# Optimization experiments

Hardware: AMD Instinct MI355X
Metric: run time of the kernel (lower is better)

## Reference

```python
import jax, jax.numpy as jnp
import numpy as np

B, C, H, W = 32, 512, 32, 32
R = C // 2  # reduced channels for key/prod projections


def setup_inputs() -> dict:
    key = jax.random.key(0)
    ks = jax.random.split(key, 8)
    s_in = 1.0 / np.sqrt(C)
    return {
        "x": jax.random.normal(ks[0], (B, C, H, W), jnp.float32),
        "Wk": jax.random.normal(ks[1], (R, C), jnp.float32) * s_in,
        "bk": jax.random.normal(ks[2], (R,), jnp.float32) * s_in,
        "Wp": jax.random.normal(ks[3], (R, C), jnp.float32) * s_in,
        "bp": jax.random.normal(ks[4], (R,), jnp.float32) * s_in,
        "Wv": jax.random.normal(ks[5], (C, C), jnp.float32) * s_in,
        "bv": jax.random.normal(ks[6], (C,), jnp.float32) * s_in,
        "param": jax.random.normal(ks[7], (1,), jnp.float32),
    }


def _conv1x1(x, Wmat, b):
    # 1x1 conv on NCHW == per-pixel channel matmul
    return jnp.einsum('bchw,oc->bohw', x, Wmat) + b[None, :, None, None]


def reference(x, Wk, bk, Wp, bp, Wv, bv, param):
    b, c, h, w = x.shape
    hw = h * w
    f_key = _conv1x1(x, Wk, bk).reshape(b, -1, hw).transpose(0, 2, 1)  # [B,HW,R]
    f_prod = _conv1x1(x, Wp, bp).reshape(b, -1, hw)                    # [B,R,HW]
    f_value = _conv1x1(x, Wv, bv).reshape(b, -1, hw)                   # [B,C,HW]
    energy = jnp.einsum('bnr,brm->bnm', f_key, f_prod)                 # [B,HW,HW]
    similarity = jax.nn.softmax(energy, axis=-1)
    # bmm(f_value, similarity^T): out[b,c,n] = sum_m f_value[b,c,m] * sim[b,n,m]
    attended = jnp.einsum('bcm,bnm->bcn', f_value, similarity).reshape(b, c, h, w)
    return x + attended * param
```

## Files before the change

kernel.cpp:

```cpp
#include <hip/hip_runtime.h>
#include <hip/hip_bf16.h>

#define BATCH 32
#define CCH   512
#define HWSZ  1024
#define RCH   256

typedef __attribute__((ext_vector_type(8))) _Float16 f16x8;
typedef __attribute__((ext_vector_type(4))) float f32x4;

__device__ __forceinline__ ushort f2h(float f) {
    _Float16 h = (_Float16)f;
    ushort u; __builtin_memcpy(&u, &h, 2);
    return u;
}
__device__ __forceinline__ float h2f(ushort u) {
    _Float16 h; __builtin_memcpy(&h, &u, 2);
    return (float)h;
}

__device__ __forceinline__ void load_lds16(const void* g, void* l) {
    __builtin_amdgcn_global_load_lds((const __attribute__((address_space(1))) void*)g,
                                     (__attribute__((address_space(3))) void*)l,
                                     16, 0, 0);
}

__device__ __forceinline__ void xcd_swizzle(int& bx, int& by, int& bz) {
    int gx = gridDim.x, gy = gridDim.y;
    int n   = gx * gy * gridDim.z;
    int lin = bx + gx * (by + gy * bz);
    int cpx = n >> 3;
    int s = (lin & 7) * cpx + (lin >> 3);
    bx = s % gx; s /= gx;
    by = s % gy;
    bz = s / gy;
}

__global__ __launch_bounds__(256) void k_pre(
    const float* __restrict__ x, ushort* __restrict__ xt,
    const float* __restrict__ Wk, const float* __restrict__ bk,
    const float* __restrict__ Wp, const float* __restrict__ bp,
    const float* __restrict__ Wv,
    ushort* __restrict__ Wkp_h, ushort* __restrict__ Wv_h, float* __restrict__ bias_kp)
{
    __shared__ float tile[64][68];
    int t = threadIdx.x;
    if (blockIdx.z == 32) {
        int base = ((blockIdx.y * 16 + blockIdx.x) * 256 + t) * 8;
        int o = base >> 9, c = base & 511;
        const float* srcKP = (o < 256) ? (Wk + (size_t)o * 512 + c)
                                       : (Wp + (size_t)(o - 256) * 512 + c);
        float4 a0 = *(const float4*)srcKP;
        float4 a1 = *(const float4*)(srcKP + 4);
        ushort4 h0, h1;
        h0.x = f2h(a0.x); h0.y = f2h(a0.y); h0.z = f2h(a0.z); h0.w = f2h(a0.w);
        h1.x = f2h(a1.x); h1.y = f2h(a1.y); h1.z = f2h(a1.z); h1.w = f2h(a1.w);
        *(ushort4*)&Wkp_h[base] = h0;
        *(ushort4*)&Wkp_h[base + 4] = h1;
        float4 v0 = *(const float4*)(Wv + base);
        float4 v1 = *(const float4*)(Wv + base + 4);
        h0.x = f2h(v0.x); h0.y = f2h(v0.y); h0.z = f2h(v0.z); h0.w = f2h(v0.w);
        h1.x = f2h(v1.x); h1.y = f2h(v1.y); h1.z = f2h(v1.z); h1.w = f2h(v1.w);
        *(ushort4*)&Wv_h[base] = h0;
        *(ushort4*)&Wv_h[base + 4] = h1;
        if (c == 0) bias_kp[o] = (o < 256) ? bk[o] : bp[o - 256];
        return;
    }
    int b  = blockIdx.z;
    int c0 = blockIdx.y * 64;
    int n0 = blockIdx.x * 64;
    const float* xb = x + (size_t)b * CCH * HWSZ;
    int tc  = t >> 4;
    int tn4 = (t & 15) * 4;
    #pragma unroll
    for (int i = 0; i < 4; ++i) {
        int c = tc + i * 16;
        *(float4*)&tile[c][tn4] = *(const float4*)&xb[(size_t)(c0 + c) * HWSZ + n0 + tn4];
    }
    __syncthreads();
    ushort* oh = xt + (size_t)b * HWSZ * CCH;
    int tn  = t >> 4;
    int tc4 = (t & 15) * 4;
    #pragma unroll
    for (int i = 0; i < 4; ++i) {
        int n = tn + i * 16;
        ushort4 h;
        h.x = f2h(tile[tc4 + 0][n]);
        h.y = f2h(tile[tc4 + 1][n]);
        h.z = f2h(tile[tc4 + 2][n]);
        h.w = f2h(tile[tc4 + 3][n]);
        *(ushort4*)&oh[(size_t)(n0 + n) * CCH + c0 + tc4] = h;
    }
}

template<int MODE>
__global__ __launch_bounds__(512, 2) void k_gemm8(
    const ushort* __restrict__ A, const ushort* __restrict__ B,
    int lda, int ldb, long aBatch, long bBatch,
    float* __restrict__ outF, ushort* __restrict__ out16,
    long oBatch, int ldo,
    const float* __restrict__ bias,
    const float* __restrict__ xres, const float* __restrict__ param,
    int NT)
{
    __shared__ ushort lds[2][2][2][8192];
    int bx = blockIdx.x, by = blockIdx.y, bz = blockIdx.z;
    xcd_swizzle(bx, by, bz);
    const int z  = bz;
    const int m0 = bx * 256;
    const int n0 = by * 256;
    const int t    = threadIdx.x;
    const int lane = t & 63;
    const int w    = t >> 6;
    const int wm = w >> 2, wn = w & 3;
    const int l15 = lane & 15;
    const int hi  = lane >> 4;
    const int G   = hi ^ ((lane >> 1) & 3);

    const ushort* Ab = A + (size_t)z * aBatch;
    const ushort* Bb = B + (size_t)z * bBatch;

    const int sr = t >> 2;
    const int sg = (t & 3) ^ ((t >> 3) & 3);

    f32x4 acc[8][4] = {};
    f16x8 a[8], b[2];

#define STAGE(par, op, ks, kt) do {                                          \
        const ushort* gb_ = (op) ? Bb : Ab;                                  \
        int ld_ = (op) ? ldb : lda;                                          \
        int r0_ = (op) ? n0 : m0;                                            \
        size_t src_ = (size_t)(r0_ + sr) * ld_ + (kt) * 64 + (ks) * 32 + sg * 8; \
        load_lds16(gb_ + src_, &lds[par][op][ks][t * 8]);                    \
        load_lds16(gb_ + src_ + (size_t)128 * ld_, &lds[par][op][ks][t * 8 + 4096]); \
    } while (0)

#define LDA_(cur, ks) do {                                                   \
        _Pragma("unroll")                                                    \
        for (int mi = 0; mi < 8; ++mi)                                       \
            a[mi] = *(const f16x8*)&lds[cur][0][ks][(wm * 128 + mi * 16 + l15) * 32 + G * 8]; \
    } while (0)

#define LDB_(cur, ks, nh) do {                                               \
        _Pragma("unroll")                                                    \
        for (int ni = 0; ni < 2; ++ni)                                       \
            b[ni] = *(const f16x8*)&lds[cur][1][ks][(wn * 64 + (nh) * 32 + ni * 16 + l15) * 32 + G * 8]; \
    } while (0)

#define BAR() __builtin_amdgcn_s_barrier()

#define WLG(N) do { asm volatile("s_waitcnt lgkmcnt(" #N ")" ::: "memory");  \
                    __builtin_amdgcn_sched_barrier(0); } while (0)

#define MM2(mi, nh) do {                                                     \
        acc[mi][(nh)*2+0] = __builtin_amdgcn_mfma_f32_16x16x32_f16(a[mi], b[0], acc[mi][(nh)*2+0], 0, 0, 0); \
        acc[mi][(nh)*2+1] = __builtin_amdgcn_mfma_f32_16x16x32_f16(a[mi], b[1], acc[mi][(nh)*2+1], 0, 0, 0); \
    } while (0)

#define MFMA_PIPE() do {                                                     \
        WLG(7); MM2(0, 0); WLG(6); MM2(1, 0); WLG(5); MM2(2, 0);             \
        WLG(4); MM2(3, 0); WLG(3); MM2(4, 0); WLG(2); MM2(5, 0);             \
        WLG(1); MM2(6, 0); WLG(0); MM2(7, 0);                                \
    } while (0)

#define MFMA_BLK1() do {                                                     \
        WLG(0);                                                              \
        MM2(0, 1); MM2(1, 1); MM2(2, 1); MM2(3, 1);                          \
        MM2(4, 1); MM2(5, 1); MM2(6, 1); MM2(7, 1);                          \
    } while (0)

    STAGE(0, 0, 0, 0); STAGE(0, 1, 0, 0); STAGE(0, 0, 1, 0); STAGE(0, 1, 1, 0);
    asm volatile("s_waitcnt vmcnt(4)" ::: "memory");
    BAR();

    for (int j = 0; j < NT - 1; ++j) {
        int cur = j & 1, nxt = cur ^ 1;
        STAGE(nxt, 0, 0, j + 1);
        LDB_(cur, 0, 0); LDA_(cur, 0);
        MFMA_PIPE();
        STAGE(nxt, 1, 0, j + 1);
        LDB_(cur, 0, 1);
        MFMA_BLK1();
        asm volatile("s_waitcnt vmcnt(4)" ::: "memory");
        BAR();
        STAGE(nxt, 0, 1, j + 1);
        LDB_(cur, 1, 0); LDA_(cur, 1);
        MFMA_PIPE();
        STAGE(nxt, 1, 1, j + 1);
        LDB_(cur, 1, 1);
        MFMA_BLK1();
        asm volatile("s_waitcnt vmcnt(4)" ::: "memory");
        BAR();
    }
    {
        int cur = (NT - 1) & 1;
        LDB_(cur, 0, 0); LDA_(cur, 0);
        MFMA_PIPE();
        LDB_(cur, 0, 1);
        MFMA_BLK1();
        asm volatile("s_waitcnt vmcnt(0)" ::: "memory");
        BAR();
        LDB_(cur, 1, 0); LDA_(cur, 1);
        MFMA_PIPE();
        LDB_(cur, 1, 1);
        MFMA_BLK1();
    }

    if (MODE == 3) {
        float* fbuf = (float*)lds;
        const float prm = param[0];
        float*       ob = outF + (size_t)z * oBatch;
        const float* xb = xres + (size_t)z * oBatch;
        #pragma unroll
        for (int h = 0; h < 2; ++h) {
            asm volatile("s_waitcnt lgkmcnt(0)" ::: "memory");
            BAR();
            if ((wn >> 1) == h) {
                #pragma unroll
                for (int mi = 0; mi < 8; ++mi)
                    #pragma unroll
                    for (int ni = 0; ni < 4; ++ni) {
                        int cc = (wn & 1) * 64 + (ni >> 1) * 32 + (ni & 1) * 16 + l15;
                        int nn = (wm * 128 + mi * 16 + hi * 4) ^ ((cc & 7) << 2);
                        *(f32x4*)&fbuf[cc * 256 + nn] = acc[mi][ni];
                    }
            }
            asm volatile("s_waitcnt lgkmcnt(0)" ::: "memory");
            BAR();
            #pragma unroll
            for (int rr = 0; rr < 16; ++rr) {
                int cc = w * 16 + rr;
                f32x4 o4 = *(const f32x4*)&fbuf[cc * 256 + ((lane * 4) ^ ((cc & 7) << 2))];
                size_t g = (size_t)(n0 + h * 128 + cc) * ldo + m0 + lane * 4;
                float4 xv = *(const float4*)&xb[g];
                float4 ov;
                ov.x = xv.x + o4[0] * prm;
                ov.y = xv.y + o4[1] * prm;
                ov.z = xv.z + o4[2] * prm;
                ov.w = xv.w + o4[3] * prm;
                *(float4*)&ob[g] = ov;
            }
        }
    } else {
        #pragma unroll
        for (int mi = 0; mi < 8; ++mi) {
            #pragma unroll
            for (int ni = 0; ni < 4; ++ni) {
                int gc  = n0 + wn * 64 + (ni >> 1) * 32 + (ni & 1) * 16 + l15;
                int gr0 = m0 + wm * 128 + mi * 16 + hi * 4;
                #pragma unroll
                for (int jj = 0; jj < 4; ++jj) {
                    int gr = gr0 + jj;
                    float v = acc[mi][ni][jj];
                    if (MODE == 0) {
                        v += bias[gc];
                        out16[(size_t)gr * ldo + gc] = f2h(v);
                    } else if (MODE == 1) {
                        v += bias[gr];
                        out16[(size_t)z * oBatch + (size_t)gr * ldo + gc] = f2h(v);
                    } else {
                        out16[(size_t)z * oBatch + (size_t)gr * ldo + gc] = f2h(v);
                    }
                }
            }
        }
    }
#undef STAGE
#undef LDA_
#undef LDB_
#undef BAR
#undef WLG
#undef MM2
#undef MFMA_PIPE
#undef MFMA_BLK1
}

__global__ __launch_bounds__(256) void k_softmax(ushort* __restrict__ E)
{
    int t    = threadIdx.x;
    int rowi = t >> 7;
    int tl   = t & 127;
    ushort* row = E + (size_t)(blockIdx.x * 2 + rowi) * HWSZ;
    uint4 u = *(const uint4*)&row[tl * 8];
    float v[8];
    v[0] = h2f(u.x & 0xffff); v[1] = h2f(u.x >> 16);
    v[2] = h2f(u.y & 0xffff); v[3] = h2f(u.y >> 16);
    v[4] = h2f(u.z & 0xffff); v[5] = h2f(u.z >> 16);
    v[6] = h2f(u.w & 0xffff); v[7] = h2f(u.w >> 16);
    float mx = v[0];
    #pragma unroll
    for (int i = 1; i < 8; ++i) mx = fmaxf(mx, v[i]);
    #pragma unroll
    for (int off = 1; off < 64; off <<= 1)
        mx = fmaxf(mx, __shfl_xor(mx, off));
    __shared__ float redm[2][2];
    __shared__ float reds[2][2];
    int lane = t & 63, wv = (t >> 6) & 1;
    if (lane == 0) redm[rowi][wv] = mx;
    __syncthreads();
    mx = fmaxf(redm[rowi][0], redm[rowi][1]);
    float s = 0.f;
    #pragma unroll
    for (int i = 0; i < 8; ++i) { v[i] = __expf(v[i] - mx); s += v[i]; }
    #pragma unroll
    for (int off = 1; off < 64; off <<= 1)
        s += __shfl_xor(s, off);
    if (lane == 0) reds[rowi][wv] = s;
    __syncthreads();
    s = reds[rowi][0] + reds[rowi][1];
    float inv = 1.0f / s;
    uint4 o;
    o.x = (unsigned)f2h(v[0] * inv) | ((unsigned)f2h(v[1] * inv) << 16);
    o.y = (unsigned)f2h(v[2] * inv) | ((unsigned)f2h(v[3] * inv) << 16);
    o.z = (unsigned)f2h(v[4] * inv) | ((unsigned)f2h(v[5] * inv) << 16);
    o.w = (unsigned)f2h(v[6] * inv) | ((unsigned)f2h(v[7] * inv) << 16);
    *(uint4*)&row[tl * 8] = o;
}

extern "C" void kernel_launch(void* const* d_in, const int* in_sizes, int n_in,
                              void* d_out, int out_size, void* d_ws, size_t ws_size,
                              hipStream_t stream)
{
    const float* x    = (const float*)d_in[0];
    const float* Wk   = (const float*)d_in[1];
    const float* bk   = (const float*)d_in[2];
    const float* Wp   = (const float*)d_in[3];
    const float* bp   = (const float*)d_in[4];
    const float* Wv   = (const float*)d_in[5];
    const float* bv   = (const float*)d_in[6];
    const float* prm  = (const float*)d_in[7];
    float* out = (float*)d_out;
    char* ws = (char*)d_ws;

    const size_t SZ16 = (size_t)BATCH * HWSZ * CCH * 2;
    ushort* xt    = (ushort*)(ws + 0);
    ushort* KPt   = (ushort*)(ws + SZ16);
    ushort* fv    = (ushort*)(ws + 2 * SZ16);
    ushort* E     = (ushort*)(ws + 3 * SZ16);
    char* wbase   = ws + 3 * SZ16 + (size_t)BATCH * HWSZ * HWSZ * 2;
    ushort* Wkp_h = (ushort*)(wbase);
    ushort* Wv_h  = (ushort*)(wbase + 524288);
    float*  bias_kp = (float*)(wbase + 2 * 524288);

    k_pre<<<dim3(16, 8, 33), 256, 0, stream>>>(
        x, xt, Wk, bk, Wp, bp, Wv, Wkp_h, Wv_h, bias_kp);

    k_gemm8<0><<<dim3(128, 2, 1), 512, 0, stream>>>(
        xt, Wkp_h, CCH, CCH, 0, 0,
        nullptr, KPt, 0, CCH,
        bias_kp, nullptr, nullptr, CCH / 64);

    k_gemm8<1><<<dim3(2, 4, 32), 512, 0, stream>>>(
        Wv_h, xt, CCH, CCH, 0, (long)HWSZ * CCH,
        nullptr, fv, (long)CCH * HWSZ, HWSZ,
        bv, nullptr, nullptr, CCH / 64);

    k_gemm8<2><<<dim3(4, 4, 32), 512, 0, stream>>>(
        KPt, KPt + RCH, CCH, CCH,
        (long)HWSZ * CCH, (long)HWSZ * CCH,
        nullptr, E, (long)HWSZ * HWSZ, HWSZ,
        nullptr, nullptr, nullptr, RCH / 64);

    k_softmax<<<BATCH * HWSZ / 2, 256, 0, stream>>>(E);

    k_gemm8<3><<<dim3(4, 2, 32), 512, 0, stream>>>(
        E, fv, HWSZ, HWSZ,
        (long)HWSZ * HWSZ, (long)CCH * HWSZ,
        out, nullptr, (long)CCH * HWSZ, HWSZ,
        nullptr, x, prm, HWSZ / 64);
}
```

Measured before the change: 179.6 us.

## Halve GEMM M-tile and K-step, single-stage double buffer, raise occupancy target

Shrinks the GEMM block tile from 256x256 to 128x256 and the K step from 64 to 32. The LDS double buffer is rebuilt as two flat slots that are read in a single pass per iteration, and the launch bounds now ask for 4 blocks per CU. All four GEMM launches double their grid, and the residual epilogue is re-tiled into four 64-column passes. The aim is more blocks and waves to fill the CUs and hide latency. The cost is lower arithmetic intensity per tile, a full vmcnt(0) wait plus a barrier every 32-wide K step, and register pressure that could force spills under the tighter bound.

```diff
diff --git a/kernel.cpp b/kernel.cpp
--- a/kernel.cpp
+++ b/kernel.cpp
@@ -94,7 +94,7 @@
 }
 
 template<int MODE>
-__global__ __launch_bounds__(512, 2) void k_gemm8(
+__global__ __launch_bounds__(512, 4) void k_gemm8(
     const ushort* __restrict__ A, const ushort* __restrict__ B,
     int lda, int ldb, long aBatch, long bBatch,
     float* __restrict__ outF, ushort* __restrict__ out16,
@@ -103,11 +103,11 @@
     const float* __restrict__ xres, const float* __restrict__ param,
     int NT)
 {
-    __shared__ ushort lds[2][2][2][8192];
+    __shared__ ushort lds[2][12288];
     int bx = blockIdx.x, by = blockIdx.y, bz = blockIdx.z;
     xcd_swizzle(bx, by, bz);
     const int z  = bz;
-    const int m0 = bx * 256;
+    const int m0 = bx * 128;
     const int n0 = by * 256;
     const int t    = threadIdx.x;
     const int lane = t & 63;
@@ -123,87 +123,60 @@
     const int sr = t >> 2;
     const int sg = (t & 3) ^ ((t >> 3) & 3);
 
-    f32x4 acc[8][4] = {};
-    f16x8 a[8], b[2];
-
-#define STAGE(par, op, ks, kt) do {                                          \
-        const ushort* gb_ = (op) ? Bb : Ab;                                  \
-        int ld_ = (op) ? ldb : lda;                                          \
-        int r0_ = (op) ? n0 : m0;                                            \
-        size_t src_ = (size_t)(r0_ + sr) * ld_ + (kt) * 64 + (ks) * 32 + sg * 8; \
-        load_lds16(gb_ + src_, &lds[par][op][ks][t * 8]);                    \
-        load_lds16(gb_ + src_ + (size_t)128 * ld_, &lds[par][op][ks][t * 8 + 4096]); \
+    f32x4 acc[4][4] = {};
+    f16x8 a[4], b01[2], b23[2];
+
+#define STAGE(slot, kt) do {                                                 \
+        size_t sa_ = (size_t)(m0 + sr) * lda + (kt) * 32 + sg * 8;           \
+        load_lds16(Ab + sa_, &lds[slot][t * 8]);                             \
+        size_t sb_ = (size_t)(n0 + sr) * ldb + (kt) * 32 + sg * 8;           \
+        load_lds16(Bb + sb_, &lds[slot][4096 + t * 8]);                      \
+        load_lds16(Bb + sb_ + (size_t)128 * ldb, &lds[slot][8192 + t * 8]);  \
     } while (0)
 
-#define LDA_(cur, ks) do {                                                   \
-        _Pragma("unroll")                                                    \
-        for (int mi = 0; mi < 8; ++mi)                                       \
-            a[mi] = *(const f16x8*)&lds[cur][0][ks][(wm * 128 + mi * 16 + l15) * 32 + G * 8]; \
-    } while (0)
-
-#define LDB_(cur, ks, nh) do {                                               \
+#define RD_ALL(slot) do {                                                    \
         _Pragma("unroll")                                                    \
         for (int ni = 0; ni < 2; ++ni)                                       \
-            b[ni] = *(const f16x8*)&lds[cur][1][ks][(wn * 64 + (nh) * 32 + ni * 16 + l15) * 32 + G * 8]; \
+            b01[ni] = *(const f16x8*)&lds[slot][4096 + (wn * 64 + ni * 16 + l15) * 32 + G * 8]; \
+        _Pragma("unroll")                                                    \
+        for (int ni = 0; ni < 2; ++ni)                                       \
+            b23[ni] = *(const f16x8*)&lds[slot][4096 + (wn * 64 + 32 + ni * 16 + l15) * 32 + G * 8]; \
+        _Pragma("unroll")                                                    \
+        for (int mi = 0; mi < 4; ++mi)                                       \
+            a[mi] = *(const f16x8*)&lds[slot][(wm * 64 + mi * 16 + l15) * 32 + G * 8]; \
     } while (0)
 
 #define BAR() __builtin_amdgcn_s_barrier()
-
 #define WLG(N) do { asm volatile("s_waitcnt lgkmcnt(" #N ")" ::: "memory");  \
                     __builtin_amdgcn_sched_barrier(0); } while (0)
-
-#define MM2(mi, nh) do {                                                     \
-        acc[mi][(nh)*2+0] = __builtin_amdgcn_mfma_f32_16x16x32_f16(a[mi], b[0], acc[mi][(nh)*2+0], 0, 0, 0); \
-        acc[mi][(nh)*2+1] = __builtin_amdgcn_mfma_f32_16x16x32_f16(a[mi], b[1], acc[mi][(nh)*2+1], 0, 0, 0); \
+#define WVM(N) asm volatile("s_waitcnt vmcnt(" #N ")" ::: "memory")
+
+#define MM4(mi) do {                                                         \
+        acc[mi][0] = __builtin_amdgcn_mfma_f32_16x16x32_f16(a[mi], b01[0], acc[mi][0], 0, 0, 0); \
+        acc[mi][1] = __builtin_amdgcn_mfma_f32_16x16x32_f16(a[mi], b01[1], acc[mi][1], 0, 0, 0); \
+        acc[mi][2] = __builtin_amdgcn_mfma_f32_16x16x32_f16(a[mi], b23[0], acc[mi][2], 0, 0, 0); \
+        acc[mi][3] = __builtin_amdgcn_mfma_f32_16x16x32_f16(a[mi], b23[1], acc[mi][3], 0, 0, 0); \
     } while (0)
 
 #define MFMA_PIPE() do {                                                     \
-        WLG(7); MM2(0, 0); WLG(6); MM2(1, 0); WLG(5); MM2(2, 0);             \
-        WLG(4); MM2(3, 0); WLG(3); MM2(4, 0); WLG(2); MM2(5, 0);             \
-        WLG(1); MM2(6, 0); WLG(0); MM2(7, 0);                                \
+        WLG(3); MM4(0); WLG(2); MM4(1); WLG(1); MM4(2); WLG(0); MM4(3);      \
     } while (0)
 
-#define MFMA_BLK1() do {                                                     \
-        WLG(0);                                                              \
-        MM2(0, 1); MM2(1, 1); MM2(2, 1); MM2(3, 1);                          \
-        MM2(4, 1); MM2(5, 1); MM2(6, 1); MM2(7, 1);                          \
-    } while (0)
-
-    STAGE(0, 0, 0, 0); STAGE(0, 1, 0, 0); STAGE(0, 0, 1, 0); STAGE(0, 1, 1, 0);
-    asm volatile("s_waitcnt vmcnt(4)" ::: "memory");
+    STAGE(0, 0);
+    WVM(0);
     BAR();
 
     for (int j = 0; j < NT - 1; ++j) {
-        int cur = j & 1, nxt = cur ^ 1;
-        STAGE(nxt, 0, 0, j + 1);
-        LDB_(cur, 0, 0); LDA_(cur, 0);
+        int cur = j & 1;
+        STAGE(cur ^ 1, j + 1);
+        RD_ALL(cur);
         MFMA_PIPE();
-        STAGE(nxt, 1, 0, j + 1);
-        LDB_(cur, 0, 1);
-        MFMA_BLK1();
-        asm volatile("s_waitcnt vmcnt(4)" ::: "memory");
+        WVM(0);
         BAR();
-        STAGE(nxt, 0, 1, j + 1);
-        LDB_(cur, 1, 0); LDA_(cur, 1);
+    }
+    {
+        RD_ALL(1);
         MFMA_PIPE();
-        STAGE(nxt, 1, 1, j + 1);
-        LDB_(cur, 1, 1);
-        MFMA_BLK1();
-        asm volatile("s_waitcnt vmcnt(4)" ::: "memory");
-        BAR();
-    }
-    {
-        int cur = (NT - 1) & 1;
-        LDB_(cur, 0, 0); LDA_(cur, 0);
-        MFMA_PIPE();
-        LDB_(cur, 0, 1);
-        MFMA_BLK1();
-        asm volatile("s_waitcnt vmcnt(0)" ::: "memory");
-        BAR();
-        LDB_(cur, 1, 0); LDA_(cur, 1);
-        MFMA_PIPE();
-        LDB_(cur, 1, 1);
-        MFMA_BLK1();
     }
 
     if (MODE == 3) {
@@ -212,26 +185,27 @@
         float*       ob = outF + (size_t)z * oBatch;
         const float* xb = xres + (size_t)z * oBatch;
         #pragma unroll
-        for (int h = 0; h < 2; ++h) {
+        for (int h = 0; h < 4; ++h) {
             asm volatile("s_waitcnt lgkmcnt(0)" ::: "memory");
             BAR();
-            if ((wn >> 1) == h) {
+            if (wn == h) {
                 #pragma unroll
-                for (int mi = 0; mi < 8; ++mi)
+                for (int mi = 0; mi < 4; ++mi)
                     #pragma unroll
                     for (int ni = 0; ni < 4; ++ni) {
-                        int cc = (wn & 1) * 64 + (ni >> 1) * 32 + (ni & 1) * 16 + l15;
-                        int nn = (wm * 128 + mi * 16 + hi * 4) ^ ((cc & 7) << 2);
-                        *(f32x4*)&fbuf[cc * 256 + nn] = acc[mi][ni];
+                        int cc = (ni >> 1) * 32 + (ni & 1) * 16 + l15;
+                        int nn = (wm * 64 + mi * 16 + hi * 4) ^ ((cc & 7) << 2);
+                        *(f32x4*)&fbuf[cc * 128 + nn] = acc[mi][ni];
                     }
             }
             asm volatile("s_waitcnt lgkmcnt(0)" ::: "memory");
             BAR();
             #pragma unroll
-            for (int rr = 0; rr < 16; ++rr) {
-                int cc = w * 16 + rr;
-                f32x4 o4 = *(const f32x4*)&fbuf[cc * 256 + ((lane * 4) ^ ((cc & 7) << 2))];
-                size_t g = (size_t)(n0 + h * 128 + cc) * ldo + m0 + lane * 4;
+            for (int rr = 0; rr < 4; ++rr) {
+                int cc  = w * 8 + rr * 2 + (lane >> 5);
+                int col = (lane & 31) * 4;
+                f32x4 o4 = *(const f32x4*)&fbuf[cc * 128 + (col ^ ((cc & 7) << 2))];
+                size_t g = (size_t)(n0 + h * 64 + cc) * ldo + m0 + col;
                 float4 xv = *(const float4*)&xb[g];
                 float4 ov;
                 ov.x = xv.x + o4[0] * prm;
@@ -243,11 +217,11 @@
         }
     } else {
         #pragma unroll
-        for (int mi = 0; mi < 8; ++mi) {
+        for (int mi = 0; mi < 4; ++mi) {
             #pragma unroll
             for (int ni = 0; ni < 4; ++ni) {
                 int gc  = n0 + wn * 64 + (ni >> 1) * 32 + (ni & 1) * 16 + l15;
-                int gr0 = m0 + wm * 128 + mi * 16 + hi * 4;
+                int gr0 = m0 + wm * 64 + mi * 16 + hi * 4;
                 #pragma unroll
                 for (int jj = 0; jj < 4; ++jj) {
                     int gr = gr0 + jj;
@@ -266,13 +240,12 @@
         }
     }
 #undef STAGE
-#undef LDA_
-#undef LDB_
+#undef RD_ALL
 #undef BAR
 #undef WLG
-#undef MM2
+#undef WVM
+#undef MM4
 #undef MFMA_PIPE
-#undef MFMA_BLK1
 }
 
 __global__ __launch_bounds__(256) void k_softmax(ushort* __restrict__ E)
@@ -345,27 +318,27 @@
     k_pre<<<dim3(16, 8, 33), 256, 0, stream>>>(
         x, xt, Wk, bk, Wp, bp, Wv, Wkp_h, Wv_h, bias_kp);
 
-    k_gemm8<0><<<dim3(128, 2, 1), 512, 0, stream>>>(
+    k_gemm8<0><<<dim3(256, 2, 1), 512, 0, stream>>>(
         xt, Wkp_h, CCH, CCH, 0, 0,
         nullptr, KPt, 0, CCH,
-        bias_kp, nullptr, nullptr, CCH / 64);
-
-    k_gemm8<1><<<dim3(2, 4, 32), 512, 0, stream>>>(
+        bias_kp, nullptr, nullptr, CCH / 32);
+
+    k_gemm8<1><<<dim3(4, 4, 32), 512, 0, stream>>>(
         Wv_h, xt, CCH, CCH, 0, (long)HWSZ * CCH,
         nullptr, fv, (long)CCH * HWSZ, HWSZ,
-        bv, nullptr, nullptr, CCH / 64);
-
-    k_gemm8<2><<<dim3(4, 4, 32), 512, 0, stream>>>(
+        bv, nullptr, nullptr, CCH / 32);
+
+    k_gemm8<2><<<dim3(8, 4, 32), 512, 0, stream>>>(
         KPt, KPt + RCH, CCH, CCH,
         (long)HWSZ * CCH, (long)HWSZ * CCH,
         nullptr, E, (long)HWSZ * HWSZ, HWSZ,
-        nullptr, nullptr, nullptr, RCH / 64);
+        nullptr, nullptr, nullptr, RCH / 32);
 
     k_softmax<<<BATCH * HWSZ / 2, 256, 0, stream>>>(E);
 
-    k_gemm8<3><<<dim3(4, 2, 32), 512, 0, stream>>>(
+    k_gemm8<3><<<dim3(8, 2, 32), 512, 0, stream>>>(
         E, fv, HWSZ, HWSZ,
         (long)HWSZ * HWSZ, (long)CCH * HWSZ,
         out, nullptr, (long)CCH * HWSZ, HWSZ,
-        nullptr, x, prm, HWSZ / 64);
-}
+        nullptr, x, prm, HWSZ / 32);
+}
```

New measurement: 179.2 us. Within noise of the previous version (-0.2%).

## Add 128x256 tile GEMM with BK=32 for projection GEMMs

Applied to the files above, without the earlier changes.

Introduces a smaller-tile GEMM kernel (128 rows x 256 cols, K step 32, about 48KB LDS, launch bounds allowing 4 blocks per CU) for the key/prod and value projection GEMMs. The grids for those launches double, which gives more workgroups to fill the CUs, and the higher occupancy target is meant to hide latency better. The existing 256x256 kernel stays in use for the energy and attended GEMMs, and its unused bias epilogue paths are trimmed. In exchange, each block reuses less data per load, more global traffic is needed per flop, and the 4-wave-per-SIMD bound limits registers per thread.

```diff
diff --git a/kernel.cpp b/kernel.cpp
--- a/kernel.cpp
+++ b/kernel.cpp
@@ -23,6 +23,10 @@
     __builtin_amdgcn_global_load_lds((const __attribute__((address_space(1))) void*)g,
                                      (__attribute__((address_space(3))) void*)l,
                                      16, 0, 0);
+}
+
+__device__ __forceinline__ f32x4 mfma16(f16x8 a, f16x8 b, f32x4 c) {
+    return __builtin_amdgcn_mfma_f32_16x16x32_f16(a, b, c, 0, 0, 0);
 }
 
 __device__ __forceinline__ void xcd_swizzle(int& bx, int& by, int& bz) {
@@ -94,12 +98,120 @@
 }
 
 template<int MODE>
-__global__ __launch_bounds__(512, 2) void k_gemm8(
+__global__ __launch_bounds__(512, 4) void k_gemm128(
+    const ushort* __restrict__ A, const ushort* __restrict__ B,
+    int lda, int ldb, long aBatch, long bBatch,
+    ushort* __restrict__ out16, long oBatch, int ldo,
+    const float* __restrict__ bias, int NT)
+{
+    __shared__ ushort lds[2][12288];
+    int bx = blockIdx.x, by = blockIdx.y, bz = blockIdx.z;
+    xcd_swizzle(bx, by, bz);
+    const int z  = bz;
+    const int m0 = bx * 128;
+    const int n0 = by * 256;
+    const int t    = threadIdx.x;
+    const int lane = t & 63;
+    const int w    = t >> 6;
+    const int wm = w >> 2, wn = w & 3;
+    const int l15 = lane & 15;
+    const int hi  = lane >> 4;
+    const int G   = hi ^ ((lane >> 1) & 3);
+
+    const ushort* Ab = A + (size_t)z * aBatch;
+    const ushort* Bb = B + (size_t)z * bBatch;
+
+    const int sr = t >> 2;
+    const int sg = (t & 3) ^ ((t >> 3) & 3);
+
+    f32x4 acc[4][4] = {};
+    f16x8 a[4], b01[2], b23[2];
+
+#define STAGE(slot, kt) do {                                                 \
+        size_t sa_ = (size_t)(m0 + sr) * lda + (kt) * 32 + sg * 8;           \
+        load_lds16(Ab + sa_, &lds[slot][t * 8]);                             \
+        size_t sb_ = (size_t)(n0 + sr) * ldb + (kt) * 32 + sg * 8;           \
+        load_lds16(Bb + sb_, &lds[slot][4096 + t * 8]);                      \
+        load_lds16(Bb + sb_ + (size_t)128 * ldb, &lds[slot][8192 + t * 8]);  \
+    } while (0)
+
+#define RD_ALL(slot) do {                                                    \
+        _Pragma("unroll")                                                    \
+        for (int ni = 0; ni < 2; ++ni)                                       \
+            b01[ni] = *(const f16x8*)&lds[slot][4096 + (wn * 64 + ni * 16 + l15) * 32 + G * 8]; \
+        _Pragma("unroll")                                                    \
+        for (int ni = 0; ni < 2; ++ni)                                       \
+            b23[ni] = *(const f16x8*)&lds[slot][4096 + (wn * 64 + 32 + ni * 16 + l15) * 32 + G * 8]; \
+        _Pragma("unroll")                                                    \
+        for (int mi = 0; mi < 4; ++mi)                                       \
+            a[mi] = *(const f16x8*)&lds[slot][(wm * 64 + mi * 16 + l15) * 32 + G * 8]; \
+    } while (0)
+
+#define BAR() __builtin_amdgcn_s_barrier()
+#define WLG(N) do { asm volatile("s_waitcnt lgkmcnt(" #N ")" ::: "memory");  \
+                    __builtin_amdgcn_sched_barrier(0); } while (0)
+#define WVM(N) asm volatile("s_waitcnt vmcnt(" #N ")" ::: "memory")
+
+#define MM4(mi) do {                                                         \
+        acc[mi][0] = mfma16(a[mi], b01[0], acc[mi][0]);                      \
+        acc[mi][1] = mfma16(a[mi], b01[1], acc[mi][1]);                      \
+        acc[mi][2] = mfma16(a[mi], b23[0], acc[mi][2]);                      \
+        acc[mi][3] = mfma16(a[mi], b23[1], acc[mi][3]);                      \
+    } while (0)
+
+#define MFMA_PIPE() do {                                                     \
+        WLG(3); MM4(0); WLG(2); MM4(1); WLG(1); MM4(2); WLG(0); MM4(3);      \
+    } while (0)
+
+    STAGE(0, 0);
+    WVM(0);
+    BAR();
+    for (int j = 0; j < NT - 1; ++j) {
+        int cur = j & 1;
+        STAGE(cur ^ 1, j + 1);
+        RD_ALL(cur);
+        MFMA_PIPE();
+        WVM(0);
+        BAR();
+    }
+    RD_ALL(1);
+    MFMA_PIPE();
+
+    #pragma unroll
+    for (int mi = 0; mi < 4; ++mi) {
+        #pragma unroll
+        for (int ni = 0; ni < 4; ++ni) {
+            int gc  = n0 + wn * 64 + (ni >> 1) * 32 + (ni & 1) * 16 + l15;
+            int gr0 = m0 + wm * 64 + mi * 16 + hi * 4;
+            #pragma unroll
+            for (int jj = 0; jj < 4; ++jj) {
+                int gr = gr0 + jj;
+                float v = acc[mi][ni][jj];
+                if (MODE == 0) {
+                    v += bias[gc];
+                    out16[(size_t)gr * ldo + gc] = f2h(v);
+                } else {
+                    v += bias[gr];
+                    out16[(size_t)z * oBatch + (size_t)gr * ldo + gc] = f2h(v);
+                }
+            }
+        }
+    }
+#undef STAGE
+#undef RD_ALL
+#undef BAR
+#undef WLG
+#undef WVM
+#undef MM4
+#undef MFMA_PIPE
+}
+
+template<int MODE>
+__global__ __launch_bounds__(512, 2) void k_gemm256(
     const ushort* __restrict__ A, const ushort* __restrict__ B,
     int lda, int ldb, long aBatch, long bBatch,
     float* __restrict__ outF, ushort* __restrict__ out16,
     long oBatch, int ldo,
-    const float* __restrict__ bias,
     const float* __restrict__ xres, const float* __restrict__ param,
     int NT)
 {
@@ -153,8 +265,8 @@
                     __builtin_amdgcn_sched_barrier(0); } while (0)
 
 #define MM2(mi, nh) do {                                                     \
-        acc[mi][(nh)*2+0] = __builtin_amdgcn_mfma_f32_16x16x32_f16(a[mi], b[0], acc[mi][(nh)*2+0], 0, 0, 0); \
-        acc[mi][(nh)*2+1] = __builtin_amdgcn_mfma_f32_16x16x32_f16(a[mi], b[1], acc[mi][(nh)*2+1], 0, 0, 0); \
+        acc[mi][(nh)*2+0] = mfma16(a[mi], b[0], acc[mi][(nh)*2+0]);          \
+        acc[mi][(nh)*2+1] = mfma16(a[mi], b[1], acc[mi][(nh)*2+1]);          \
     } while (0)
 
 #define MFMA_PIPE() do {                                                     \
@@ -251,16 +363,8 @@
                 #pragma unroll
                 for (int jj = 0; jj < 4; ++jj) {
                     int gr = gr0 + jj;
-                    float v = acc[mi][ni][jj];
-                    if (MODE == 0) {
-                        v += bias[gc];
-                        out16[(size_t)gr * ldo + gc] = f2h(v);
-                    } else if (MODE == 1) {
-                        v += bias[gr];
-                        out16[(size_t)z * oBatch + (size_t)gr * ldo + gc] = f2h(v);
-                    } else {
-                        out16[(size_t)z * oBatch + (size_t)gr * ldo + gc] = f2h(v);
-                    }
+                    out16[(size_t)z * oBatch + (size_t)(gr0 + jj) * ldo + gc] = f2h(acc[mi][ni][jj]);
+                    (void)gr;
                 }
             }
         }
@@ -345,27 +449,25 @@
     k_pre<<<dim3(16, 8, 33), 256, 0, stream>>>(
         x, xt, Wk, bk, Wp, bp, Wv, Wkp_h, Wv_h, bias_kp);
 
-    k_gemm8<0><<<dim3(128, 2, 1), 512, 0, stream>>>(
+    k_gemm128<0><<<dim3(256, 2, 1), 512, 0, stream>>>(
         xt, Wkp_h, CCH, CCH, 0, 0,
-        nullptr, KPt, 0, CCH,
-        bias_kp, nullptr, nullptr, CCH / 64);
-
-    k_gemm8<1><<<dim3(2, 4, 32), 512, 0, stream>>>(
+        KPt, 0, CCH, bias_kp, CCH / 32);
+
+    k_gemm128<1><<<dim3(4, 4, 32), 512, 0, stream>>>(
         Wv_h, xt, CCH, CCH, 0, (long)HWSZ * CCH,
-        nullptr, fv, (long)CCH * HWSZ, HWSZ,
-        bv, nullptr, nullptr, CCH / 64);
-
-    k_gemm8<2><<<dim3(4, 4, 32), 512, 0, stream>>>(
+        fv, (long)CCH * HWSZ, HWSZ, bv, CCH / 32);
+
+    k_gemm256<2><<<dim3(4, 4, 32), 512, 0, stream>>>(
         KPt, KPt + RCH, CCH, CCH,
         (long)HWSZ * CCH, (long)HWSZ * CCH,
         nullptr, E, (long)HWSZ * HWSZ, HWSZ,
-        nullptr, nullptr, nullptr, RCH / 64);
+        nullptr, nullptr, RCH / 64);
 
     k_softmax<<<BATCH * HWSZ / 2, 256, 0, stream>>>(E);
 
-    k_gemm8<3><<<dim3(4, 2, 32), 512, 0, stream>>>(
+    k_gemm256<3><<<dim3(4, 2, 32), 512, 0, stream>>>(
         E, fv, HWSZ, HWSZ,
         (long)HWSZ * HWSZ, (long)CCH * HWSZ,
         out, nullptr, (long)CCH * HWSZ, HWSZ,
-        nullptr, x, prm, HWSZ / 64);
-}
+        x, prm, HWSZ / 64);
+}
```

Result: no change. 176.7 us (-1.6%).
